# Performance work log

Hardware: AMD Instinct MI355X
Metric: run time of the kernel (lower is better)

## Reference

```python
import jax, jax.numpy as jnp
import numpy as np
from jax.ops import segment_sum, segment_max

N, E, C, L = 50000, 600000, 128, 4
H = 2 * C  # GENConv MLP hidden = expansion(2) * in_channels
EPS_MSG = 1e-7   # GENConv message eps
EPS_LN = 1e-5    # PyG LayerNorm eps (graph mode)
EPS_GN = 1e-5    # GraphNorm eps
EPS_SM = 1e-16   # PyG softmax denominator eps


def setup_inputs() -> dict:
    key = jax.random.key(0)
    ks = jax.random.split(key, 8)
    s = 0.05
    return dict(
        x=jax.random.normal(ks[0], (N, C), jnp.float32),
        src=jax.random.randint(ks[1], (E,), 0, N),
        dst=jax.random.randint(ks[2], (E,), 0, N),
        W1=jax.random.normal(ks[3], (L, C, H), jnp.float32) * s,
        b1=jnp.zeros((L, H), jnp.float32),
        ln_w=jnp.ones((L, H), jnp.float32),
        ln_b=jnp.zeros((L, H), jnp.float32),
        W2=jax.random.normal(ks[4], (L, H, C), jnp.float32) * s,
        b2=jnp.zeros((L, C), jnp.float32),
        t=jnp.ones((L,), jnp.float32),      # learn_t=True, init t=1.0
        gn_w=jnp.ones((L, C), jnp.float32),
        gn_b=jnp.zeros((L, C), jnp.float32),
        gn_a=jnp.ones((L, C), jnp.float32),  # GraphNorm mean_scale
        lin_w=jax.random.normal(ks[5], (C, 1), jnp.float32) * s,
        lin_b=jnp.zeros((1,), jnp.float32),
    )


def graph_norm(x, w, b, a):
    # single graph: per-channel mean over nodes
    mean = x.mean(axis=0)
    out = x - a * mean
    var = (out * out).mean(axis=0)
    return w * out / jnp.sqrt(var + EPS_GN) + b


def gen_conv(x, src, dst, t, W1, b1, ln_w, ln_b, W2, b2):
    # message: relu(x_j) + eps  (no edge_attr)
    msg = jax.nn.relu(x[src]) + EPS_MSG           # [E, C]
    z = t * msg
    m = segment_max(z, dst, num_segments=N)        # [N, C]
    ex = jnp.exp(z - m[dst])
    den = segment_sum(ex, dst, num_segments=N) + EPS_SM
    alpha = ex / den[dst]                          # per-node per-channel softmax
    agg = segment_sum(msg * alpha, dst, num_segments=N)  # [N, C]
    out = agg + x                                  # root add
    # MLP([C, 2C, C]) with PyG LayerNorm (graph mode) + ReLU between layers
    h = out @ W1 + b1                              # [N, H]
    h = (h - h.mean()) / (h.std() + EPS_LN)        # graph-mode LN: scalar stats
    h = jax.nn.relu(h * ln_w + ln_b)
    return h @ W2 + b2                             # [N, C]


def reference(x, src, dst, W1, b1, ln_w, ln_b, W2, b2, t, gn_w, gn_b, gn_a, lin_w, lin_b):
    for l in range(L):
        # DeepGCNLayer block='res+': norm -> act -> (dropout=0) -> conv, residual add
        h = graph_norm(x, gn_w[l], gn_b[l], gn_a[l])
        h = jax.nn.relu(h)
        h = gen_conv(h, src, dst, t[l], W1[l], b1[l], ln_w[l], ln_b[l], W2[l], b2[l])
        x = x + h
    return x @ lin_w + lin_b                       # [N, 1]
```

## Files before the change

kernel.cpp:

```cpp
#include <hip/hip_runtime.h>

#define C_DIM 128
#define H_DIM 256
#define L_NUM 4

typedef __attribute__((ext_vector_type(8))) short bf16x8;
typedef __attribute__((ext_vector_type(4))) float f32x4;

__device__ __forceinline__ unsigned short f2bf(float f){
  unsigned u = __builtin_bit_cast(unsigned, f);
  u = u + 0x7FFFu + ((u >> 16) & 1u);
  return (unsigned short)(u >> 16);
}
__device__ __forceinline__ float bf2f(unsigned short b){
  return __builtin_bit_cast(float, ((unsigned)b) << 16);
}
__device__ __forceinline__ float fexp2(float x){
#if __has_builtin(__builtin_amdgcn_exp2f)
  return __builtin_amdgcn_exp2f(x);
#else
  float r; asm("v_exp_f32 %0, %1" : "=v"(r) : "v"(x)); return r;
#endif
}

__global__ void k_pre(const float* __restrict__ W1, const float* __restrict__ W2,
                      unsigned short* __restrict__ W1t, unsigned short* __restrict__ W2t,
                      const float* __restrict__ X, float* __restrict__ part, int NB,
                      const int* __restrict__ dst, int* __restrict__ cnt,
                      int N, int E, int S0){
  __shared__ float a1[256], a2[256];
  int b = blockIdx.x;
  if (b < 512){
    int i = b*256 + threadIdx.x;
    int l = i >> 15, r = i & 32767;
    { int k = r >> 8, n = r & 255;  W1t[l*32768 + n*128 + k] = f2bf(W1[i]); }
    { int k = r >> 7, n = r & 127;  W2t[l*32768 + n*256 + k] = f2bf(W2[i]); }
  } else if (b < 512 + S0){
    int chunk = b - 512;
    int t = threadIdx.x; int c = t & 127; int half = t >> 7;
    int r0 = chunk*128, rend = min(r0 + 128, N);
    float sa=0.f,sb=0.f,sc=0.f,sd=0.f, qa=0.f,qb=0.f,qc=0.f,qd=0.f;
    int r = r0 + half;
    for (; r + 6 < rend; r += 8){
      float v0 = X[(size_t)r*C_DIM + c];
      float v1 = X[(size_t)(r+2)*C_DIM + c];
      float v2 = X[(size_t)(r+4)*C_DIM + c];
      float v3 = X[(size_t)(r+6)*C_DIM + c];
      sa += v0; qa = fmaf(v0, v0, qa);
      sb += v1; qb = fmaf(v1, v1, qb);
      sc += v2; qc = fmaf(v2, v2, qc);
      sd += v3; qd = fmaf(v3, v3, qd);
    }
    for (; r < rend; r += 2){
      float v = X[(size_t)r*C_DIM + c];
      sa += v; qa = fmaf(v, v, qa);
    }
    float s = (sa + sb) + (sc + sd);
    float s2 = (qa + qb) + (qc + qd);
    a1[t] = s; a2[t] = s2; __syncthreads();
    if (t < 128){
      part[t*NB + chunk]       = a1[t] + a1[t+128];
      part[(128+t)*NB + chunk] = a2[t] + a2[t+128];
    }
  } else {
    int nb = gridDim.x - 512 - S0;
    int bb = b - 512 - S0;
    for (int e = bb*256 + threadIdx.x; e < E; e += nb*256)
      atomicAdd(cnt + dst[e], 1);
  }
}

__global__ void k_scan_local(const int* __restrict__ cnt, int* __restrict__ rp,
                             int* __restrict__ bsum, int N){
  __shared__ int tmp[256];
  int t = threadIdx.x; int i = blockIdx.x*256 + t;
  int v = (i < N) ? cnt[i] : 0;
  tmp[t] = v; __syncthreads();
  for (int off = 1; off < 256; off <<= 1){
    int x = (t >= off) ? tmp[t-off] : 0; __syncthreads();
    tmp[t] += x; __syncthreads();
  }
  if (i < N) rp[i] = tmp[t] - v;
  if (t == 255) bsum[blockIdx.x] = tmp[t];
}

__global__ void k_scan_bsums(const int* __restrict__ bsum, int* __restrict__ boff, int nb){
  __shared__ int tmp[256];
  int t = threadIdx.x;
  int v = (t < nb) ? bsum[t] : 0;
  tmp[t] = v; __syncthreads();
  for (int off = 1; off < 256; off <<= 1){
    int x = (t >= off) ? tmp[t-off] : 0; __syncthreads();
    tmp[t] += x; __syncthreads();
  }
  if (t < nb) boff[t] = tmp[t] - v;
}

__global__ void k_scan_add(int* __restrict__ rp, const int* __restrict__ boff,
                           int* __restrict__ cnt, int N, int E){
  int i = blockIdx.x*256 + threadIdx.x;
  if (i < N){ rp[i] += boff[blockIdx.x]; cnt[i] = 0; }
  if (i == 0) rp[N] = E;
}

__global__ void k_scatter(const int* __restrict__ src, const int* __restrict__ dst,
                          const int* __restrict__ rp, int* __restrict__ cnt,
                          int* __restrict__ csrc, int E){
  for (int e = blockIdx.x*blockDim.x + threadIdx.x; e < E; e += gridDim.x*blockDim.x){
    int d = dst[e];
    int pos = rp[d] + atomicAdd(cnt + d, 1);
    csrc[pos] = src[e];
  }
}

__global__ void k_gn_coef(const float* __restrict__ part, int NB, int nb,
                          const float* __restrict__ gw, const float* __restrict__ gb,
                          const float* __restrict__ ga, const float* __restrict__ tptr, int l,
                          float* __restrict__ coef, int N){
  int c = blockIdx.x;
  int t = threadIdx.x;
  float s = 0.f, s2 = 0.f;
  for (int i = t; i < nb; i += 256){
    s  += part[c*NB + i];
    s2 += part[(128+c)*NB + i];
  }
  __shared__ float sh1[256], sh2[256];
  sh1[t] = s; sh2[t] = s2; __syncthreads();
  for (int off = 128; off; off >>= 1){
    if (t < off){ sh1[t] += sh1[t+off]; sh2[t] += sh2[t+off]; }
    __syncthreads();
  }
  if (t == 0){
    float kk = tptr[l] * 1.4426950408889634f;
    float inv = 1.f/(float)N;
    float mean = sh1[0]*inv;
    float am = ga[c]*mean;
    float var = sh2[0]*inv - 2.f*am*mean + am*am;
    float scale = gw[c] * rsqrtf(var + 1e-5f);
    coef[c] = scale * kk;
    coef[128+c] = (gb[c] - scale*am) * kk;
  }
}

__global__ void k_gpre(const float* __restrict__ X, const float* __restrict__ coef,
                       unsigned* __restrict__ G2, int total4){
  int i = blockIdx.x*blockDim.x + threadIdx.x;
  if (i >= total4) return;
  int c4 = i & 31;
  float4 x = ((const float4*)X)[i];
  float4 A = ((const float4*)coef)[c4];
  float4 B = ((const float4*)coef)[32 + c4];
  float o0 = fmaxf(A.x*x.x + B.x, 0.f);
  float o1 = fmaxf(A.y*x.y + B.y, 0.f);
  float o2 = fmaxf(A.z*x.z + B.z, 0.f);
  float o3 = fmaxf(A.w*x.w + B.w, 0.f);
  uint2 pk = make_uint2((unsigned)f2bf(o0) | ((unsigned)f2bf(o1) << 16),
                        (unsigned)f2bf(o2) | ((unsigned)f2bf(o3) << 16));
  ((uint2*)G2)[i] = pk;
}

__global__ void k_agg(const unsigned* __restrict__ G, const int* __restrict__ rp,
                      const int* __restrict__ csrc, const float* __restrict__ tptr, int l,
                      unsigned short* __restrict__ U, int N){
  int wave = threadIdx.x >> 6, lane = threadIdx.x & 63;
  int n = blockIdx.x*2 + wave;
  if (n >= N) return;
  float invkk = 1.f / (tptr[l] * 1.4426950408889634f);
  int jb = __builtin_amdgcn_readfirstlane(rp[n]);
  int je = __builtin_amdgcn_readfirstlane(rp[n+1]);
  float dA0=0.f,dA1=0.f,sA0=0.f,sA1=0.f;
  float dB0=0.f,dB1=0.f,sB0=0.f,sB1=0.f;
  unsigned uo = G[(size_t)n*64 + lane];

  #define EDGEA(uu) { \
    float p0 = __builtin_bit_cast(float, (uu) << 16); \
    float p1 = __builtin_bit_cast(float, (uu) & 0xffff0000u); \
    float e0 = fexp2(p0); float e1 = fexp2(p1); \
    dA0 += e0; dA1 += e1; \
    sA0 = fmaf(p0, e0, sA0); sA1 = fmaf(p1, e1, sA1); }
  #define EDGEB(uu) { \
    float p0 = __builtin_bit_cast(float, (uu) << 16); \
    float p1 = __builtin_bit_cast(float, (uu) & 0xffff0000u); \
    float e0 = fexp2(p0); float e1 = fexp2(p1); \
    dB0 += e0; dB1 += e1; \
    sB0 = fmaf(p0, e0, sB0); sB1 = fmaf(p1, e1, sB1); }

  int j = jb;
  for (; j + 7 < je; j += 8){
    int i0 = csrc[j+0], i1 = csrc[j+1], i2 = csrc[j+2], i3 = csrc[j+3];
    int i4 = csrc[j+4], i5 = csrc[j+5], i6 = csrc[j+6], i7 = csrc[j+7];
    unsigned v0 = G[(size_t)i0*64 + lane];
    unsigned v1 = G[(size_t)i1*64 + lane];
    unsigned v2 = G[(size_t)i2*64 + lane];
    unsigned v3 = G[(size_t)i3*64 + lane];
    unsigned v4 = G[(size_t)i4*64 + lane];
    unsigned v5 = G[(size_t)i5*64 + lane];
    unsigned v6 = G[(size_t)i6*64 + lane];
    unsigned v7 = G[(size_t)i7*64 + lane];
    EDGEA(v0); EDGEB(v1); EDGEA(v2); EDGEB(v3);
    EDGEA(v4); EDGEB(v5); EDGEA(v6); EDGEB(v7);
  }
  for (; j + 3 < je; j += 4){
    int i0 = csrc[j+0], i1 = csrc[j+1], i2 = csrc[j+2], i3 = csrc[j+3];
    unsigned v0 = G[(size_t)i0*64 + lane];
    unsigned v1 = G[(size_t)i1*64 + lane];
    unsigned v2 = G[(size_t)i2*64 + lane];
    unsigned v3 = G[(size_t)i3*64 + lane];
    EDGEA(v0); EDGEB(v1); EDGEA(v2); EDGEB(v3);
  }
  for (; j < je; ++j){
    int i0 = csrc[j];
    unsigned v0 = G[(size_t)i0*64 + lane];
    EDGEA(v0);
  }
  #undef EDGEA
  #undef EDGEB

  float d0 = dA0 + dB0, d1 = dA1 + dB1;
  float s0 = sA0 + sB0, s1 = sA1 + sB1;
  float o0 = __builtin_bit_cast(float, uo << 16);
  float o1 = __builtin_bit_cast(float, uo & 0xffff0000u);
  float u0 = invkk * (s0/(d0 + 1e-16f) + o0) + 1e-7f;
  float u1 = invkk * (s1/(d1 + 1e-16f) + o1) + 1e-7f;
  unsigned pk = (unsigned)f2bf(u0) | ((unsigned)f2bf(u1) << 16);
  *(unsigned*)(U + n*C_DIM + lane*2) = pk;
}

__global__ void k_gemm1(const unsigned short* __restrict__ A, const unsigned short* __restrict__ Bt,
                        const float* __restrict__ b1, unsigned short* __restrict__ H1,
                        float* __restrict__ part, int M){
  __shared__ __align__(16) char smem[64*256];
  __shared__ float rbuf[8];
  const int tid = threadIdx.x;
  const int m0 = blockIdx.x * 64;
  const int wave = tid >> 6, lane = tid & 63;
  const int lr = lane & 15, lc = lane >> 4;

  bf16x8 bf[4][4];
  #pragma unroll
  for (int nf = 0; nf < 4; ++nf){
    int n = wave*64 + nf*16 + lr;
    #pragma unroll
    for (int ks = 0; ks < 4; ++ks)
      bf[nf][ks] = *(const bf16x8*)(Bt + n*128 + ks*32 + lc*8);
  }
  #pragma unroll
  for (int p = 0; p < 4; ++p){
    int idx = p*256 + tid;
    int row = idx >> 4, ch = idx & 15;
    int r = m0 + row;
    uint4 v = make_uint4(0u,0u,0u,0u);
    if (r < M) v = *(const uint4*)(A + r*128 + ch*8);
    int o = (row*256 + ch*16) ^ ((row & 7) << 4);
    *(uint4*)(smem + o) = v;
  }
  __syncthreads();

  f32x4 acc[4][4] = {};
  #pragma unroll
  for (int ks = 0; ks < 4; ++ks){
    bf16x8 a[4];
    #pragma unroll
    for (int mf = 0; mf < 4; ++mf){
      int row = mf*16 + lr;
      int o = (row*256 + ks*64 + lc*16) ^ ((row & 7) << 4);
      a[mf] = *(const bf16x8*)(smem + o);
    }
    #pragma unroll
    for (int mf = 0; mf < 4; ++mf)
      #pragma unroll
      for (int nf = 0; nf < 4; ++nf)
        acc[mf][nf] = __builtin_amdgcn_mfma_f32_16x16x32_bf16(a[mf], bf[nf][ks], acc[mf][nf], 0, 0, 0);
  }

  float s1 = 0.f, s2 = 0.f;
  #pragma unroll
  for (int mf = 0; mf < 4; ++mf){
    #pragma unroll
    for (int j = 0; j < 4; ++j){
      int r = m0 + mf*16 + lc*4 + j;
      if (r < M){
        #pragma unroll
        for (int nf = 0; nf < 4; ++nf){
          int col = wave*64 + nf*16 + lr;
          float v = acc[mf][nf][j] + b1[col];
          H1[r*H_DIM + col] = f2bf(v);
          s1 += v; s2 += v*v;
        }
      }
    }
  }
  #pragma unroll
  for (int o = 32; o; o >>= 1){ s1 += __shfl_down(s1, o); s2 += __shfl_down(s2, o); }
  if (lane == 0){ rbuf[wave] = s1; rbuf[4 + wave] = s2; }
  __syncthreads();
  if (tid == 0)
    part[blockIdx.x*2]     = rbuf[0]+rbuf[1]+rbuf[2]+rbuf[3];
  if (tid == 1)
    part[blockIdx.x*2 + 1] = rbuf[4]+rbuf[5]+rbuf[6]+rbuf[7];
}

__global__ void k_gemm2(const unsigned short* __restrict__ H1,
                        const float* __restrict__ lnpart, int nparts,
                        const float* __restrict__ lnw, const float* __restrict__ lnb,
                        const unsigned short* __restrict__ Bt, const float* __restrict__ b2,
                        const float* __restrict__ Xin, float* __restrict__ Xout,
                        float* __restrict__ part, int NB,
                        const float* __restrict__ lw, const float* __restrict__ lb,
                        float* __restrict__ out, int M){
  __shared__ __align__(16) char smem[64*512];
  __shared__ float red1[256], red2[256];
  __shared__ float colw[256], colb[256];
  __shared__ float rowdot[64];
  const int tid = threadIdx.x;
  const int m0 = blockIdx.x * 64;
  const int wave = tid >> 6, lane = tid & 63;
  const int lr = lane & 15, lc = lane >> 4;
  const bool last = (lw != nullptr);

  {
    float s1 = 0.f, s2 = 0.f;
    for (int i = tid; i < nparts; i += 256){ s1 += lnpart[2*i]; s2 += lnpart[2*i+1]; }
    red1[tid] = s1; red2[tid] = s2; __syncthreads();
    for (int o = 128; o; o >>= 1){
      if (tid < o){ red1[tid] += red1[tid+o]; red2[tid] += red2[tid+o]; }
      __syncthreads();
    }
    double NH = (double)M * (double)H_DIM;
    double mean = (double)red1[0] / NH;
    double var = (double)red2[0] / NH - mean*mean;
    double sd = sqrt(var > 0.0 ? var : 0.0);
    float denom = (float)sd + 1e-5f;
    float wv = lnw[tid] / denom;
    colw[tid] = wv;
    colb[tid] = lnb[tid] - (float)mean * wv;
    if (tid < 64) rowdot[tid] = 0.f;
    __syncthreads();
  }

  bf16x8 bf[2][8];
  #pragma unroll
  for (int nf = 0; nf < 2; ++nf){
    int n = wave*32 + nf*16 + lr;
    #pragma unroll
    for (int ks = 0; ks < 8; ++ks)
      bf[nf][ks] = *(const bf16x8*)(Bt + n*256 + ks*32 + lc*8);
  }
  #pragma unroll
  for (int p = 0; p < 8; ++p){
    int idx = (p*256 + tid)*8;
    int row = idx >> 8, col = idx & 255;
    int r = m0 + row;
    uint4 v = make_uint4(0u,0u,0u,0u);
    if (r < M) v = *(const uint4*)(H1 + r*H_DIM + col);
    unsigned short hb[8] = {(unsigned short)(v.x&0xffff),(unsigned short)(v.x>>16),
                            (unsigned short)(v.y&0xffff),(unsigned short)(v.y>>16),
                            (unsigned short)(v.z&0xffff),(unsigned short)(v.z>>16),
                            (unsigned short)(v.w&0xffff),(unsigned short)(v.w>>16)};
    unsigned outp[4];
    #pragma unroll
    for (int q = 0; q < 4; ++q){
      float f0 = fmaxf(colw[col+2*q]  *bf2f(hb[2*q])   + colb[col+2*q],   0.f);
      float f1 = fmaxf(colw[col+2*q+1]*bf2f(hb[2*q+1]) + colb[col+2*q+1], 0.f);
      outp[q] = (unsigned)f2bf(f0) | ((unsigned)f2bf(f1) << 16);
    }
    int o = (row*512 + col*2) ^ ((row & 7) << 4);
    *(uint4*)(smem + o) = make_uint4(outp[0],outp[1],outp[2],outp[3]);
  }
  __syncthreads();

  f32x4 acc[4][2] = {};
  #pragma unroll
  for (int ks = 0; ks < 8; ++ks){
    bf16x8 a[4];
    #pragma unroll
    for (int mf = 0; mf < 4; ++mf){
      int row = mf*16 + lr;
      int o = (row*512 + ks*64 + lc*16) ^ ((row & 7) << 4);
      a[mf] = *(const bf16x8*)(smem + o);
    }
    #pragma unroll
    for (int mf = 0; mf < 4; ++mf)
      #pragma unroll
      for (int nf = 0; nf < 2; ++nf)
        acc[mf][nf] = __builtin_amdgcn_mfma_f32_16x16x32_bf16(a[mf], bf[nf][ks], acc[mf][nf], 0, 0, 0);
  }

  float sA[2] = {0.f, 0.f}, sB[2] = {0.f, 0.f};
  #pragma unroll
  for (int mf = 0; mf < 4; ++mf){
    #pragma unroll
    for (int j = 0; j < 4; ++j){
      int r = m0 + mf*16 + lc*4 + j;
      if (r < M){
        float p = 0.f;
        #pragma unroll
        for (int nf = 0; nf < 2; ++nf){
          int col = wave*32 + nf*16 + lr;
          float v = Xin[r*C_DIM + col] + acc[mf][nf][j] + b2[col];
          if (!last){
            Xout[r*C_DIM + col] = v;
            sA[nf] += v; sB[nf] += v*v;
          } else {
            p += v * lw[col];
          }
        }
        if (last){
          p += __shfl_xor(p, 1); p += __shfl_xor(p, 2);
          p += __shfl_xor(p, 4); p += __shfl_xor(p, 8);
          if (lr == 0) atomicAdd(&rowdot[r - m0], p);
        }
      }
    }
  }
  if (!last){
    #pragma unroll
    for (int nf = 0; nf < 2; ++nf){
      sA[nf] += __shfl_xor(sA[nf], 16); sA[nf] += __shfl_xor(sA[nf], 32);
      sB[nf] += __shfl_xor(sB[nf], 16); sB[nf] += __shfl_xor(sB[nf], 32);
    }
    if (lane < 16){
      #pragma unroll
      for (int nf = 0; nf < 2; ++nf){
        int col = wave*32 + nf*16 + lr;
        part[col*NB + blockIdx.x]       = sA[nf];
        part[(128+col)*NB + blockIdx.x] = sB[nf];
      }
    }
  } else {
    __syncthreads();
    if (tid < 64 && m0 + tid < M) out[m0 + tid] = rowdot[tid] + lb[0];
  }
}

extern "C" void kernel_launch(void* const* d_in, const int* in_sizes, int n_in,
                              void* d_out, int out_size, void* d_ws, size_t ws_size,
                              hipStream_t stream){
  const float* x    = (const float*)d_in[0];
  const int*   src  = (const int*)d_in[1];
  const int*   dst  = (const int*)d_in[2];
  const float* W1   = (const float*)d_in[3];
  const float* b1   = (const float*)d_in[4];
  const float* lnw  = (const float*)d_in[5];
  const float* lnb  = (const float*)d_in[6];
  const float* W2   = (const float*)d_in[7];
  const float* b2   = (const float*)d_in[8];
  const float* tpt  = (const float*)d_in[9];
  const float* gnw  = (const float*)d_in[10];
  const float* gnb  = (const float*)d_in[11];
  const float* gna  = (const float*)d_in[12];
  const float* linw = (const float*)d_in[13];
  const float* linb = (const float*)d_in[14];
  (void)n_in; (void)out_size; (void)ws_size;
  const int N = in_sizes[0] / C_DIM;
  const int E = in_sizes[1];
  float* out = (float*)d_out;

  const int gmw = (N + 63)/64;
  const int S0  = (N + 127)/128;
  const int NB  = gmw;

  char* wsp = (char*)d_ws; size_t off = 0;
  auto alloc = [&](size_t b)->char*{ char* p = wsp + off; off += (b + 255) & ~(size_t)255; return p; };
  int* cnt          = (int*)alloc((size_t)N*4);
  int* rp           = (int*)alloc((size_t)(N+1)*4);
  int* bsum         = (int*)alloc(1024);
  int* boff         = (int*)alloc(1024);
  float* gncoef     = (float*)alloc(1024);
  float* lnpart     = (float*)alloc((size_t)gmw*2*4);
  float* part       = (float*)alloc((size_t)NB*256*4);
  int* csrc         = (int*)alloc((size_t)E*4);
  unsigned short* W1t = (unsigned short*)alloc((size_t)L_NUM*C_DIM*H_DIM*2);
  unsigned short* W2t = (unsigned short*)alloc((size_t)L_NUM*C_DIM*H_DIM*2);
  unsigned* g       = (unsigned*)alloc((size_t)N*C_DIM*2);
  unsigned short* U = (unsigned short*)alloc((size_t)N*C_DIM*2);
  unsigned short* h1 = (unsigned short*)alloc((size_t)N*H_DIM*2);
  float* xc         = (float*)alloc((size_t)N*C_DIM*4);

  const int SB = (N + 255)/256;
  hipMemsetAsync(cnt, 0, (size_t)N*4, stream);
  k_pre<<<512 + S0 + 1024, 256, 0, stream>>>(W1, W2, W1t, W2t, x, part, NB, dst, cnt, N, E, S0);
  k_scan_local<<<SB, 256, 0, stream>>>(cnt, rp, bsum, N);
  k_scan_bsums<<<1, 256, 0, stream>>>(bsum, boff, SB);
  k_scan_add<<<SB, 256, 0, stream>>>(rp, boff, cnt, N, E);
  k_scatter<<<1024, 256, 0, stream>>>(src, dst, rp, cnt, csrc, E);

  for (int l = 0; l < L_NUM; ++l){
    int nb = (l == 0) ? S0 : gmw;
    const float* Xin = (l == 0) ? x : xc;
    bool lastL = (l == L_NUM - 1);
    k_gn_coef<<<128, 256, 0, stream>>>(part, NB, nb, gnw + l*C_DIM, gnb + l*C_DIM, gna + l*C_DIM, tpt, l, gncoef, N);
    k_gpre<<<(N*32 + 255)/256, 256, 0, stream>>>(Xin, gncoef, g, N*32);
    k_agg<<<(N + 1)/2, 128, 0, stream>>>(g, rp, csrc, tpt, l, U, N);
    k_gemm1<<<gmw, 256, 0, stream>>>(U, W1t + (size_t)l*C_DIM*H_DIM, b1 + l*H_DIM, h1, lnpart, N);
    k_gemm2<<<gmw, 256, 0, stream>>>(h1, lnpart, gmw, lnw + l*H_DIM, lnb + l*H_DIM,
                                     W2t + (size_t)l*C_DIM*H_DIM, b2 + l*C_DIM,
                                     Xin, xc, part, NB,
                                     lastL ? linw : nullptr, linb, out, N);
  }
}
```

Baseline: 410.2 us.

## Fuse neighbor softmax aggregation into first MLP GEMM kernel

Merges the per-node softmax aggregation kernel into the first GEMM kernel. Each wave aggregates 16 nodes and writes the bf16 results directly into the swizzled shared-memory A tile, so the intermediate U buffer and one launch per layer go away. In exchange, far fewer waves run the latency-bound gather, with each wave processing nodes sequentially, which reduces memory-level parallelism. Some index arithmetic is also widened to size_t.

```diff
diff --git a/kernel.cpp b/kernel.cpp
--- a/kernel.cpp
+++ b/kernel.cpp
@@ -159,18 +159,17 @@
   ((uint2*)G2)[i] = pk;
 }
 
-__global__ void k_agg(const unsigned* __restrict__ G, const int* __restrict__ rp,
-                      const int* __restrict__ csrc, const float* __restrict__ tptr, int l,
-                      unsigned short* __restrict__ U, int N){
-  int wave = threadIdx.x >> 6, lane = threadIdx.x & 63;
-  int n = blockIdx.x*2 + wave;
-  if (n >= N) return;
-  float invkk = 1.f / (tptr[l] * 1.4426950408889634f);
-  int jb = __builtin_amdgcn_readfirstlane(rp[n]);
-  int je = __builtin_amdgcn_readfirstlane(rp[n+1]);
-  float dA0=0.f,dA1=0.f,sA0=0.f,sA1=0.f;
-  float dB0=0.f,dB1=0.f,sB0=0.f,sB1=0.f;
-  unsigned uo = G[(size_t)n*64 + lane];
+__global__ void k_agg_gemm1(const unsigned* __restrict__ G, const int* __restrict__ rp,
+                            const int* __restrict__ csrc, const float* __restrict__ tptr, int l,
+                            const unsigned short* __restrict__ Bt, const float* __restrict__ b1,
+                            unsigned short* __restrict__ H1, float* __restrict__ part, int N){
+  __shared__ __align__(16) char smem[64*256];
+  __shared__ float rbuf[8];
+  const int tid = threadIdx.x;
+  const int m0 = blockIdx.x * 64;
+  const int wave = tid >> 6, lane = tid & 63;
+  const int lr = lane & 15, lc = lane >> 4;
+  const float invkk = 1.f / (tptr[l] * 1.4426950408889634f);
 
   #define EDGEA(uu) { \
     float p0 = __builtin_bit_cast(float, (uu) << 16); \
@@ -185,56 +184,56 @@
     dB0 += e0; dB1 += e1; \
     sB0 = fmaf(p0, e0, sB0); sB1 = fmaf(p1, e1, sB1); }
 
-  int j = jb;
-  for (; j + 7 < je; j += 8){
-    int i0 = csrc[j+0], i1 = csrc[j+1], i2 = csrc[j+2], i3 = csrc[j+3];
-    int i4 = csrc[j+4], i5 = csrc[j+5], i6 = csrc[j+6], i7 = csrc[j+7];
-    unsigned v0 = G[(size_t)i0*64 + lane];
-    unsigned v1 = G[(size_t)i1*64 + lane];
-    unsigned v2 = G[(size_t)i2*64 + lane];
-    unsigned v3 = G[(size_t)i3*64 + lane];
-    unsigned v4 = G[(size_t)i4*64 + lane];
-    unsigned v5 = G[(size_t)i5*64 + lane];
-    unsigned v6 = G[(size_t)i6*64 + lane];
-    unsigned v7 = G[(size_t)i7*64 + lane];
-    EDGEA(v0); EDGEB(v1); EDGEA(v2); EDGEB(v3);
-    EDGEA(v4); EDGEB(v5); EDGEA(v6); EDGEB(v7);
-  }
-  for (; j + 3 < je; j += 4){
-    int i0 = csrc[j+0], i1 = csrc[j+1], i2 = csrc[j+2], i3 = csrc[j+3];
-    unsigned v0 = G[(size_t)i0*64 + lane];
-    unsigned v1 = G[(size_t)i1*64 + lane];
-    unsigned v2 = G[(size_t)i2*64 + lane];
-    unsigned v3 = G[(size_t)i3*64 + lane];
-    EDGEA(v0); EDGEB(v1); EDGEA(v2); EDGEB(v3);
-  }
-  for (; j < je; ++j){
-    int i0 = csrc[j];
-    unsigned v0 = G[(size_t)i0*64 + lane];
-    EDGEA(v0);
+  for (int i = 0; i < 16; ++i){
+    int row = wave*16 + i;
+    int n = m0 + row;
+    unsigned pk = 0u;
+    if (n < N){
+      int jb = __builtin_amdgcn_readfirstlane(rp[n]);
+      int je = __builtin_amdgcn_readfirstlane(rp[n+1]);
+      float dA0=0.f,dA1=0.f,sA0=0.f,sA1=0.f;
+      float dB0=0.f,dB1=0.f,sB0=0.f,sB1=0.f;
+      unsigned uo = G[(size_t)n*64 + lane];
+      int j = jb;
+      for (; j + 7 < je; j += 8){
+        int i0 = csrc[j+0], i1 = csrc[j+1], i2 = csrc[j+2], i3 = csrc[j+3];
+        int i4 = csrc[j+4], i5 = csrc[j+5], i6 = csrc[j+6], i7 = csrc[j+7];
+        unsigned v0 = G[(size_t)i0*64 + lane];
+        unsigned v1 = G[(size_t)i1*64 + lane];
+        unsigned v2 = G[(size_t)i2*64 + lane];
+        unsigned v3 = G[(size_t)i3*64 + lane];
+        unsigned v4 = G[(size_t)i4*64 + lane];
+        unsigned v5 = G[(size_t)i5*64 + lane];
+        unsigned v6 = G[(size_t)i6*64 + lane];
+        unsigned v7 = G[(size_t)i7*64 + lane];
+        EDGEA(v0); EDGEB(v1); EDGEA(v2); EDGEB(v3);
+        EDGEA(v4); EDGEB(v5); EDGEA(v6); EDGEB(v7);
+      }
+      for (; j + 3 < je; j += 4){
+        int i0 = csrc[j+0], i1 = csrc[j+1], i2 = csrc[j+2], i3 = csrc[j+3];
+        unsigned v0 = G[(size_t)i0*64 + lane];
+        unsigned v1 = G[(size_t)i1*64 + lane];
+        unsigned v2 = G[(size_t)i2*64 + lane];
+        unsigned v3 = G[(size_t)i3*64 + lane];
+        EDGEA(v0); EDGEB(v1); EDGEA(v2); EDGEB(v3);
+      }
+      for (; j < je; ++j){
+        unsigned v0 = G[(size_t)csrc[j]*64 + lane];
+        EDGEA(v0);
+      }
+      float d0 = dA0 + dB0, d1 = dA1 + dB1;
+      float s0 = sA0 + sB0, s1 = sA1 + sB1;
+      float o0 = __builtin_bit_cast(float, uo << 16);
+      float o1 = __builtin_bit_cast(float, uo & 0xffff0000u);
+      float u0 = invkk * (s0/(d0 + 1e-16f) + o0) + 1e-7f;
+      float u1 = invkk * (s1/(d1 + 1e-16f) + o1) + 1e-7f;
+      pk = (unsigned)f2bf(u0) | ((unsigned)f2bf(u1) << 16);
+    }
+    *(unsigned*)(smem + ((row*256 + lane*4) ^ ((row & 7) << 4))) = pk;
   }
   #undef EDGEA
   #undef EDGEB
-
-  float d0 = dA0 + dB0, d1 = dA1 + dB1;
-  float s0 = sA0 + sB0, s1 = sA1 + sB1;
-  float o0 = __builtin_bit_cast(float, uo << 16);
-  float o1 = __builtin_bit_cast(float, uo & 0xffff0000u);
-  float u0 = invkk * (s0/(d0 + 1e-16f) + o0) + 1e-7f;
-  float u1 = invkk * (s1/(d1 + 1e-16f) + o1) + 1e-7f;
-  unsigned pk = (unsigned)f2bf(u0) | ((unsigned)f2bf(u1) << 16);
-  *(unsigned*)(U + n*C_DIM + lane*2) = pk;
-}
-
-__global__ void k_gemm1(const unsigned short* __restrict__ A, const unsigned short* __restrict__ Bt,
-                        const float* __restrict__ b1, unsigned short* __restrict__ H1,
-                        float* __restrict__ part, int M){
-  __shared__ __align__(16) char smem[64*256];
-  __shared__ float rbuf[8];
-  const int tid = threadIdx.x;
-  const int m0 = blockIdx.x * 64;
-  const int wave = tid >> 6, lane = tid & 63;
-  const int lr = lane & 15, lc = lane >> 4;
+  __syncthreads();
 
   bf16x8 bf[4][4];
   #pragma unroll
@@ -244,18 +243,6 @@
     for (int ks = 0; ks < 4; ++ks)
       bf[nf][ks] = *(const bf16x8*)(Bt + n*128 + ks*32 + lc*8);
   }
-  #pragma unroll
-  for (int p = 0; p < 4; ++p){
-    int idx = p*256 + tid;
-    int row = idx >> 4, ch = idx & 15;
-    int r = m0 + row;
-    uint4 v = make_uint4(0u,0u,0u,0u);
-    if (r < M) v = *(const uint4*)(A + r*128 + ch*8);
-    int o = (row*256 + ch*16) ^ ((row & 7) << 4);
-    *(uint4*)(smem + o) = v;
-  }
-  __syncthreads();
-
   f32x4 acc[4][4] = {};
   #pragma unroll
   for (int ks = 0; ks < 4; ++ks){
@@ -279,12 +266,12 @@
     #pragma unroll
     for (int j = 0; j < 4; ++j){
       int r = m0 + mf*16 + lc*4 + j;
-      if (r < M){
+      if (r < N){
         #pragma unroll
         for (int nf = 0; nf < 4; ++nf){
           int col = wave*64 + nf*16 + lr;
           float v = acc[mf][nf][j] + b1[col];
-          H1[r*H_DIM + col] = f2bf(v);
+          H1[(size_t)r*H_DIM + col] = f2bf(v);
           s1 += v; s2 += v*v;
         }
       }
@@ -352,7 +339,7 @@
     int row = idx >> 8, col = idx & 255;
     int r = m0 + row;
     uint4 v = make_uint4(0u,0u,0u,0u);
-    if (r < M) v = *(const uint4*)(H1 + r*H_DIM + col);
+    if (r < M) v = *(const uint4*)(H1 + (size_t)r*H_DIM + col);
     unsigned short hb[8] = {(unsigned short)(v.x&0xffff),(unsigned short)(v.x>>16),
                             (unsigned short)(v.y&0xffff),(unsigned short)(v.y>>16),
                             (unsigned short)(v.z&0xffff),(unsigned short)(v.z>>16),
@@ -397,9 +384,9 @@
         #pragma unroll
         for (int nf = 0; nf < 2; ++nf){
           int col = wave*32 + nf*16 + lr;
-          float v = Xin[r*C_DIM + col] + acc[mf][nf][j] + b2[col];
+          float v = Xin[(size_t)r*C_DIM + col] + acc[mf][nf][j] + b2[col];
           if (!last){
-            Xout[r*C_DIM + col] = v;
+            Xout[(size_t)r*C_DIM + col] = v;
             sA[nf] += v; sB[nf] += v*v;
           } else {
             p += v * lw[col];
@@ -473,7 +460,6 @@
   unsigned short* W1t = (unsigned short*)alloc((size_t)L_NUM*C_DIM*H_DIM*2);
   unsigned short* W2t = (unsigned short*)alloc((size_t)L_NUM*C_DIM*H_DIM*2);
   unsigned* g       = (unsigned*)alloc((size_t)N*C_DIM*2);
-  unsigned short* U = (unsigned short*)alloc((size_t)N*C_DIM*2);
   unsigned short* h1 = (unsigned short*)alloc((size_t)N*H_DIM*2);
   float* xc         = (float*)alloc((size_t)N*C_DIM*4);
 
@@ -491,8 +477,8 @@
     bool lastL = (l == L_NUM - 1);
     k_gn_coef<<<128, 256, 0, stream>>>(part, NB, nb, gnw + l*C_DIM, gnb + l*C_DIM, gna + l*C_DIM, tpt, l, gncoef, N);
     k_gpre<<<(N*32 + 255)/256, 256, 0, stream>>>(Xin, gncoef, g, N*32);
-    k_agg<<<(N + 1)/2, 128, 0, stream>>>(g, rp, csrc, tpt, l, U, N);
-    k_gemm1<<<gmw, 256, 0, stream>>>(U, W1t + (size_t)l*C_DIM*H_DIM, b1 + l*H_DIM, h1, lnpart, N);
+    k_agg_gemm1<<<gmw, 256, 0, stream>>>(g, rp, csrc, tpt, l,
+                                         W1t + (size_t)l*C_DIM*H_DIM, b1 + l*H_DIM, h1, lnpart, N);
     k_gemm2<<<gmw, 256, 0, stream>>>(h1, lnpart, gmw, lnw + l*H_DIM, lnb + l*H_DIM,
                                      W2t + (size_t)l*C_DIM*H_DIM, b2 + l*C_DIM,
                                      Xin, xc, part, NB,
```

Measured after the change: 446.0 us. 8.7% more time.
